# Optimization experiments

Hardware: AMD Instinct MI355X
Metric: run time of the kernel (lower is better)

The kernel has to match this reference:

```python
import jax, jax.numpy as jnp
import numpy as np

ALPHA = 20.0 / 100.0  # dt / tau
ONE_MINUS_ALPHA = 1.0 - ALPHA


def setup_inputs() -> dict:
    key = jax.random.key(0)
    k1, k2, k3 = jax.random.split(key, 3)
    T, B, I, H = 512, 128, 256, 512
    x = jax.random.normal(k1, (T, B, I), dtype=jnp.float32)
    hidden = jnp.zeros((B, H), dtype=jnp.float32)
    # torch Linear weights: [out_features, in_features], scaled like kaiming-uniform-ish
    W_in = jax.random.normal(k2, (H, I), dtype=jnp.float32) / np.sqrt(I)
    W_hh = jax.random.normal(k3, (H, H), dtype=jnp.float32) / np.sqrt(H)
    return {"x": x, "hidden": hidden, "W_in": W_in, "W_hh": W_hh}


def reference(x, hidden, W_in, W_hh):
    # Precompute input projection for all timesteps in one big matmul: [T,B,H]
    xin = jnp.einsum("tbi,hi->tbh", x, W_in)

    def step(h, xin_t):
        pre = xin_t + h @ W_hh.T  # [B,H]
        h_new = jax.nn.relu(h * ONE_MINUS_ALPHA + pre * ALPHA)
        return h_new, h_new

    h_final, output = jax.lax.scan(step, hidden, xin)
    return output, h_final
```

## Files before the change

kernel.cpp:

```cpp
#include <hip/hip_runtime.h>

typedef _Float16 half8 __attribute__((ext_vector_type(8)));
typedef float f32x4 __attribute__((ext_vector_type(4)));

#define NT 512
#define NB 128
#define NI 256
#define NH 512
#define NG 8
#define NS 8
#define FLAG_STRIDE 16

__global__ void w_transform(const float* __restrict__ Whh,
                            const float* __restrict__ Win,
                            _Float16* __restrict__ Wf_hh,
                            _Float16* __restrict__ Wf_in,
                            int* __restrict__ flags) {
  int tid = blockIdx.x * blockDim.x + threadIdx.x;
  if (tid < 32768) {
    int l = tid & 63, b = tid >> 6;
    int tk = b & 15, tn = b >> 4;
    int n = tn * 16 + (l & 15);
    int k = tk * 32 + (l >> 4) * 8;
    const float* src = Whh + (size_t)n * NH + k;
    _Float16* dst = Wf_hh + (size_t)tid * 8;
#pragma unroll
    for (int j = 0; j < 8; ++j) dst[j] = (_Float16)src[j];
  } else if (tid < 32768 + 16384) {
    int t2 = tid - 32768;
    int l = t2 & 63, b = t2 >> 6;
    int tk = b & 7, tn = b >> 3;
    int n = tn * 16 + (l & 15);
    int k = tk * 32 + (l >> 4) * 8;
    const float* src = Win + (size_t)n * NI + k;
    _Float16* dst = Wf_in + (size_t)t2 * 8;
#pragma unroll
    for (int j = 0; j < 8; ++j) dst[j] = (_Float16)src[j];
  } else if (tid < 32768 + 16384 + NG * NS * FLAG_STRIDE) {
    flags[tid - 32768 - 16384] = 0;
  }
}

__global__ __launch_bounds__(256)
void input_proj(const float* __restrict__ x,
                const _Float16* __restrict__ Wf_in,
                float* __restrict__ xin) {
  int lane = threadIdx.x & 63;
  int wv = threadIdx.x >> 6;
  int m0 = blockIdx.x * 16;
  int c = lane & 15, q = lane >> 4;
  int row = m0 + c;

  f32x4 acc[8];
#pragma unroll
  for (int i = 0; i < 8; ++i) acc[i] = (f32x4){0.f, 0.f, 0.f, 0.f};

#pragma unroll
  for (int kc = 0; kc < 8; ++kc) {
    const float4* ap = (const float4*)(x + (size_t)row * NI + kc * 32 + q * 8);
    float4 a0 = ap[0], a1 = ap[1];
    half8 a;
    a[0] = (_Float16)a0.x; a[1] = (_Float16)a0.y;
    a[2] = (_Float16)a0.z; a[3] = (_Float16)a0.w;
    a[4] = (_Float16)a1.x; a[5] = (_Float16)a1.y;
    a[6] = (_Float16)a1.z; a[7] = (_Float16)a1.w;
#pragma unroll
    for (int nt = 0; nt < 8; ++nt) {
      int tn = wv * 8 + nt;
      const half8* bp =
          (const half8*)(Wf_in + (((size_t)(tn * 8 + kc)) * 64 + lane) * 8);
      acc[nt] = __builtin_amdgcn_mfma_f32_16x16x32_f16(a, *bp, acc[nt], 0, 0, 0);
    }
  }
#pragma unroll
  for (int nt = 0; nt < 8; ++nt) {
    int n = wv * 128 + nt * 16 + c;
#pragma unroll
    for (int r = 0; r < 4; ++r) {
      int m = q * 4 + r;
      xin[(size_t)(m0 + m) * NH + n] = acc[nt][r];
    }
  }
}

__global__ __launch_bounds__(256, 1)
void recurrence(float* __restrict__ dout,
                const float* __restrict__ h0,
                const _Float16* __restrict__ Wf,
                _Float16* __restrict__ hbuf,
                int* __restrict__ flags) {
  __shared__ _Float16 h_sh[16][520];
  __shared__ _Float16 h16s[16][72];

  int g = blockIdx.x >> 3, s = blockIdx.x & 7;
  int tid = threadIdx.x, lane = tid & 63, wv = tid >> 6;
  int c = lane & 15, q = lane >> 4;
  int m0 = g * 16;
  int n0 = s * 64;
  int ncol = wv * 16 + c;

  int nt_global = s * 4 + wv;
  half8 bfrag[16];
#pragma unroll
  for (int kc = 0; kc < 16; ++kc)
    bfrag[kc] =
        *(const half8*)(Wf + (((size_t)(nt_global * 16 + kc)) * 64 + lane) * 8);

  float h32r[4];
#pragma unroll
  for (int r = 0; r < 4; ++r)
    h32r[r] = h0[(size_t)(m0 + q * 4 + r) * NH + n0 + ncol];

  for (int i = tid; i < 16 * 512; i += 256) {
    int m = i >> 9, n = i & 511;
    h_sh[m][n] = (_Float16)h0[(size_t)(m0 + m) * NH + n];
  }
  __syncthreads();

  int* fbase = flags + g * NS * FLAG_STRIDE;
  unsigned long long* hb64 = (unsigned long long*)hbuf;

  int cm = tid >> 4, cc = tid & 15;

#pragma unroll 1
  for (int t = 0; t < NT; ++t) {
    const float* xp = dout + ((size_t)t * NB + m0) * NH + n0;
    float xv[4];
#pragma unroll
    for (int r = 0; r < 4; ++r) xv[r] = xp[(size_t)(q * 4 + r) * NH + ncol];

    f32x4 acc0 = (f32x4){0.f, 0.f, 0.f, 0.f};
    f32x4 acc1 = (f32x4){0.f, 0.f, 0.f, 0.f};
#pragma unroll
    for (int kc = 0; kc < 16; kc += 2) {
      half8 a0 = *(const half8*)&h_sh[c][kc * 32 + q * 8];
      half8 a1 = *(const half8*)&h_sh[c][(kc + 1) * 32 + q * 8];
      acc0 = __builtin_amdgcn_mfma_f32_16x16x32_f16(a0, bfrag[kc], acc0, 0, 0, 0);
      acc1 = __builtin_amdgcn_mfma_f32_16x16x32_f16(a1, bfrag[kc + 1], acc1, 0, 0, 0);
    }

#pragma unroll
    for (int r = 0; r < 4; ++r) {
      int m = q * 4 + r;
      float hn = 0.8f * h32r[r] + 0.2f * (xv[r] + acc0[r] + acc1[r]);
      hn = fmaxf(hn, 0.f);
      h32r[r] = hn;
      dout[((size_t)t * NB + m0 + m) * NH + n0 + ncol] = hn;
      h16s[m][ncol] = (_Float16)hn;
      if (t == NT - 1)
        dout[(size_t)NT * NB * NH + (size_t)(m0 + m) * NH + n0 + ncol] = hn;
    }
    if (t == NT - 1) break;

    __syncthreads();

    {
      unsigned long long v = *(const unsigned long long*)&h16s[cm][cc * 4];
      __hip_atomic_store(
          hb64 + ((((size_t)(t & 1) * NB + m0 + cm) * NH + n0 + cc * 4) >> 2),
          v, __ATOMIC_RELAXED, __HIP_MEMORY_SCOPE_AGENT);
    }
    __syncthreads();

    if (tid == 0)
      __hip_atomic_store(&fbase[s * FLAG_STRIDE], t + 1, __ATOMIC_RELAXED,
                         __HIP_MEMORY_SCOPE_AGENT);
    if (wv == 0 && lane < NS) {
      while (__hip_atomic_load(&fbase[lane * FLAG_STRIDE], __ATOMIC_RELAXED,
                               __HIP_MEMORY_SCOPE_AGENT) < t + 1) {
      }
    }
    __syncthreads();

    {
      const unsigned long long* hb =
          hb64 + ((((size_t)(t & 1) * NB + m0) * NH) >> 2);
      unsigned long long v[8];
#pragma unroll
      for (int j = 0; j < 8; ++j) {
        int k = tid + j * 256;
        v[j] = __hip_atomic_load(hb + k, __ATOMIC_RELAXED,
                                 __HIP_MEMORY_SCOPE_AGENT);
      }
#pragma unroll
      for (int j = 0; j < 8; ++j) {
        int k = tid + j * 256;
        int m = k >> 7, o = k & 127;
        *(unsigned long long*)&h_sh[m][o * 4] = v[j];
      }
    }
    __syncthreads();
  }
}

extern "C" void kernel_launch(void* const* d_in, const int* in_sizes, int n_in,
                              void* d_out, int out_size, void* d_ws,
                              size_t ws_size, hipStream_t stream) {
  const float* x      = (const float*)d_in[0];
  const float* hidden = (const float*)d_in[1];
  const float* W_in   = (const float*)d_in[2];
  const float* W_hh   = (const float*)d_in[3];
  float* out = (float*)d_out;

  _Float16* Wf_hh = (_Float16*)d_ws;
  _Float16* Wf_in = Wf_hh + (size_t)NH * NH;
  _Float16* hbuf  = Wf_in;
  int* flags = (int*)((char*)d_ws + (size_t)NH * NH * 2 + (size_t)NH * NI * 2);

  w_transform<<<196, 256, 0, stream>>>(W_hh, W_in, Wf_hh, Wf_in, flags);
  input_proj<<<(NT * NB) / 16, 256, 0, stream>>>(x, Wf_in, out);

  void* args[] = {(void*)&out, (void*)&hidden, (void*)&Wf_hh, (void*)&hbuf,
                  (void*)&flags};
  hipLaunchCooperativeKernel((void*)recurrence, dim3(NG * NS), dim3(256), args,
                             0, stream);
}
```

Before: 1.353 ms.

## Split recurrence across block pairs and overlap partner exchange with local MFMA half

The recurrence now uses 16 blocks of 512 threads, so each batch group is handled by a pair of blocks that each own half the hidden columns, replacing groups of eight blocks. Each step first runs the MFMAs over the block's own half of h, which is already in shared memory, then waits on the partner's flag and pulls only the partner's half through a column-major exchange buffer. This cuts the number of blocks that must synchronise per step and hides part of the flag wait behind local compute. In exchange, each block holds twice as many weight fragments in registers and does more work per step, with fewer blocks active overall.

```diff
diff --git a/kernel.cpp b/kernel.cpp
--- a/kernel.cpp
+++ b/kernel.cpp
@@ -7,8 +7,6 @@
 #define NB 128
 #define NI 256
 #define NH 512
-#define NG 8
-#define NS 8
 #define FLAG_STRIDE 16
 
 __global__ void w_transform(const float* __restrict__ Whh,
@@ -36,7 +34,7 @@
     _Float16* dst = Wf_in + (size_t)t2 * 8;
 #pragma unroll
     for (int j = 0; j < 8; ++j) dst[j] = (_Float16)src[j];
-  } else if (tid < 32768 + 16384 + NG * NS * FLAG_STRIDE) {
+  } else if (tid < 32768 + 16384 + 256) {
     flags[tid - 32768 - 16384] = 0;
   }
 }
@@ -83,113 +81,139 @@
   }
 }
 
-__global__ __launch_bounds__(256, 1)
+__global__ __launch_bounds__(512, 2)
 void recurrence(float* __restrict__ dout,
                 const float* __restrict__ h0,
                 const _Float16* __restrict__ Wf,
-                _Float16* __restrict__ hbuf,
+                unsigned long long* __restrict__ hbuf64,
                 int* __restrict__ flags) {
   __shared__ _Float16 h_sh[16][520];
-  __shared__ _Float16 h16s[16][72];
-
-  int g = blockIdx.x >> 3, s = blockIdx.x & 7;
+
+  int g = blockIdx.x >> 1, s = blockIdx.x & 1;
   int tid = threadIdx.x, lane = tid & 63, wv = tid >> 6;
   int c = lane & 15, q = lane >> 4;
   int m0 = g * 16;
-  int n0 = s * 64;
-  int ncol = wv * 16 + c;
-
-  int nt_global = s * 4 + wv;
-  half8 bfrag[16];
-#pragma unroll
-  for (int kc = 0; kc < 16; ++kc)
-    bfrag[kc] =
-        *(const half8*)(Wf + (((size_t)(nt_global * 16 + kc)) * 64 + lane) * 8);
-
-  float h32r[4];
-#pragma unroll
-  for (int r = 0; r < 4; ++r)
-    h32r[r] = h0[(size_t)(m0 + q * 4 + r) * NH + n0 + ncol];
-
-  for (int i = tid; i < 16 * 512; i += 256) {
-    int m = i >> 9, n = i & 511;
-    h_sh[m][n] = (_Float16)h0[(size_t)(m0 + m) * NH + n];
-  }
+  int sc = s * 256;
+  int P0 = 256 - sc;
+
+  int ntg = s * 16 + wv * 2;
+  half8 bfrag[2][16];
+#pragma unroll
+  for (int nt = 0; nt < 2; ++nt) {
+#pragma unroll
+    for (int kk = 0; kk < 16; ++kk) {
+      int kcg = (kk < 8) ? (s * 8 + kk) : ((8 - s * 8) + (kk - 8));
+      bfrag[nt][kk] =
+          *(const half8*)(Wf + (((size_t)(ntg + nt) * 16 + kcg) * 64 + lane) * 8);
+    }
+  }
+
+  float h32r[2][4];
+#pragma unroll
+  for (int nt = 0; nt < 2; ++nt)
+#pragma unroll
+    for (int r = 0; r < 4; ++r)
+      h32r[nt][r] =
+          h0[(size_t)(m0 + q * 4 + r) * NH + sc + wv * 32 + nt * 16 + c];
+
+  for (int i = tid; i < 16 * 512; i += 512)
+    h_sh[i >> 9][i & 511] = (_Float16)h0[(size_t)(m0 + (i >> 9)) * NH + (i & 511)];
   __syncthreads();
 
-  int* fbase = flags + g * NS * FLAG_STRIDE;
-  unsigned long long* hb64 = (unsigned long long*)hbuf;
-
-  int cm = tid >> 4, cc = tid & 15;
+  unsigned short* hsb = (unsigned short*)&h_sh[0][0];
+  int* fbase = flags + g * 2 * FLAG_STRIDE;
+  int* myflag = fbase + s * FLAG_STRIDE;
+  int* pflag  = fbase + (1 - s) * FLAG_STRIDE;
 
 #pragma unroll 1
   for (int t = 0; t < NT; ++t) {
-    const float* xp = dout + ((size_t)t * NB + m0) * NH + n0;
-    float xv[4];
-#pragma unroll
-    for (int r = 0; r < 4; ++r) xv[r] = xp[(size_t)(q * 4 + r) * NH + ncol];
-
-    f32x4 acc0 = (f32x4){0.f, 0.f, 0.f, 0.f};
-    f32x4 acc1 = (f32x4){0.f, 0.f, 0.f, 0.f};
-#pragma unroll
-    for (int kc = 0; kc < 16; kc += 2) {
-      half8 a0 = *(const half8*)&h_sh[c][kc * 32 + q * 8];
-      half8 a1 = *(const half8*)&h_sh[c][(kc + 1) * 32 + q * 8];
-      acc0 = __builtin_amdgcn_mfma_f32_16x16x32_f16(a0, bfrag[kc], acc0, 0, 0, 0);
-      acc1 = __builtin_amdgcn_mfma_f32_16x16x32_f16(a1, bfrag[kc + 1], acc1, 0, 0, 0);
-    }
-
-#pragma unroll
-    for (int r = 0; r < 4; ++r) {
-      int m = q * 4 + r;
-      float hn = 0.8f * h32r[r] + 0.2f * (xv[r] + acc0[r] + acc1[r]);
-      hn = fmaxf(hn, 0.f);
-      h32r[r] = hn;
-      dout[((size_t)t * NB + m0 + m) * NH + n0 + ncol] = hn;
-      h16s[m][ncol] = (_Float16)hn;
-      if (t == NT - 1)
-        dout[(size_t)NT * NB * NH + (size_t)(m0 + m) * NH + n0 + ncol] = hn;
-    }
-    if (t == NT - 1) break;
-
+    const float* xp = dout + ((size_t)t * NB + m0) * NH + sc;
+    float xv[2][4];
+#pragma unroll
+    for (int nt = 0; nt < 2; ++nt)
+#pragma unroll
+      for (int r = 0; r < 4; ++r)
+        xv[nt][r] = xp[(size_t)(q * 4 + r) * NH + wv * 32 + nt * 16 + c];
+
+    f32x4 acc[2][2];
+#pragma unroll
+    for (int nt = 0; nt < 2; ++nt) {
+      acc[nt][0] = (f32x4){0.f, 0.f, 0.f, 0.f};
+      acc[nt][1] = (f32x4){0.f, 0.f, 0.f, 0.f};
+    }
+#pragma unroll
+    for (int kk = 0; kk < 8; ++kk) {
+      int kcg = s * 8 + kk;
+      half8 a = *(const half8*)&h_sh[c][kcg * 32 + q * 8];
+#pragma unroll
+      for (int nt = 0; nt < 2; ++nt)
+        acc[nt][kk & 1] = __builtin_amdgcn_mfma_f32_16x16x32_f16(
+            a, bfrag[nt][kk], acc[nt][kk & 1], 0, 0, 0);
+    }
+
+    if (t > 0) {
+      while (__hip_atomic_load(pflag, __ATOMIC_RELAXED,
+                               __HIP_MEMORY_SCOPE_AGENT) < t) {
+      }
+      const unsigned long long* pb =
+          hbuf64 + ((size_t)((t - 1) & 1) * NH + P0) * 32 + (m0 >> 2);
+#pragma unroll
+      for (int j = 0; j < 2; ++j) {
+        int k = tid + j * 512;
+        int col = k >> 2, rq = k & 3;
+        unsigned long long v = __hip_atomic_load(
+            pb + (size_t)col * 32 + rq, __ATOMIC_RELAXED,
+            __HIP_MEMORY_SCOPE_AGENT);
+#pragma unroll
+        for (int i = 0; i < 4; ++i)
+          hsb[(size_t)(rq * 4 + i) * 520 + P0 + col] =
+              (unsigned short)(v >> (16 * i));
+      }
+    }
     __syncthreads();
 
-    {
-      unsigned long long v = *(const unsigned long long*)&h16s[cm][cc * 4];
-      __hip_atomic_store(
-          hb64 + ((((size_t)(t & 1) * NB + m0 + cm) * NH + n0 + cc * 4) >> 2),
-          v, __ATOMIC_RELAXED, __HIP_MEMORY_SCOPE_AGENT);
-    }
+#pragma unroll
+    for (int kk = 8; kk < 16; ++kk) {
+      int kcg = (8 - s * 8) + (kk - 8);
+      half8 a = *(const half8*)&h_sh[c][kcg * 32 + q * 8];
+#pragma unroll
+      for (int nt = 0; nt < 2; ++nt)
+        acc[nt][kk & 1] = __builtin_amdgcn_mfma_f32_16x16x32_f16(
+            a, bfrag[nt][kk], acc[nt][kk & 1], 0, 0, 0);
+    }
+
+    bool last = (t == NT - 1);
+    int slotw = t & 1;
+#pragma unroll
+    for (int nt = 0; nt < 2; ++nt) {
+      int ng = sc + wv * 32 + nt * 16 + c;
+      unsigned long long pk = 0;
+#pragma unroll
+      for (int r = 0; r < 4; ++r) {
+        int m = q * 4 + r;
+        float hn = 0.8f * h32r[nt][r] +
+                   0.2f * (xv[nt][r] + acc[nt][0][r] + acc[nt][1][r]);
+        hn = fmaxf(hn, 0.f);
+        h32r[nt][r] = hn;
+        dout[((size_t)t * NB + m0 + m) * NH + ng] = hn;
+        union { _Float16 h; unsigned short u; } cv;
+        cv.h = (_Float16)hn;
+        pk |= (unsigned long long)cv.u << (16 * r);
+        if (!last) h_sh[m][ng] = cv.h;
+        if (last)
+          dout[(size_t)NT * NB * NH + (size_t)(m0 + m) * NH + ng] = hn;
+      }
+      if (!last)
+        __hip_atomic_store(
+            hbuf64 + ((size_t)slotw * NH + ng) * 32 + (m0 >> 2) + q, pk,
+            __ATOMIC_RELAXED, __HIP_MEMORY_SCOPE_AGENT);
+    }
+    if (last) break;
+
     __syncthreads();
-
     if (tid == 0)
-      __hip_atomic_store(&fbase[s * FLAG_STRIDE], t + 1, __ATOMIC_RELAXED,
+      __hip_atomic_store(myflag, t + 1, __ATOMIC_RELAXED,
                          __HIP_MEMORY_SCOPE_AGENT);
-    if (wv == 0 && lane < NS) {
-      while (__hip_atomic_load(&fbase[lane * FLAG_STRIDE], __ATOMIC_RELAXED,
-                               __HIP_MEMORY_SCOPE_AGENT) < t + 1) {
-      }
-    }
-    __syncthreads();
-
-    {
-      const unsigned long long* hb =
-          hb64 + ((((size_t)(t & 1) * NB + m0) * NH) >> 2);
-      unsigned long long v[8];
-#pragma unroll
-      for (int j = 0; j < 8; ++j) {
-        int k = tid + j * 256;
-        v[j] = __hip_atomic_load(hb + k, __ATOMIC_RELAXED,
-                                 __HIP_MEMORY_SCOPE_AGENT);
-      }
-#pragma unroll
-      for (int j = 0; j < 8; ++j) {
-        int k = tid + j * 256;
-        int m = k >> 7, o = k & 127;
-        *(unsigned long long*)&h_sh[m][o * 4] = v[j];
-      }
-    }
-    __syncthreads();
   }
 }
 
@@ -204,7 +228,7 @@
 
   _Float16* Wf_hh = (_Float16*)d_ws;
   _Float16* Wf_in = Wf_hh + (size_t)NH * NH;
-  _Float16* hbuf  = Wf_in;
+  unsigned long long* hbuf = (unsigned long long*)Wf_in;
   int* flags = (int*)((char*)d_ws + (size_t)NH * NH * 2 + (size_t)NH * NI * 2);
 
   w_transform<<<196, 256, 0, stream>>>(W_hh, W_in, Wf_hh, Wf_in, flags);
@@ -212,6 +236,6 @@
 
   void* args[] = {(void*)&out, (void*)&hidden, (void*)&Wf_hh, (void*)&hbuf,
                   (void*)&flags};
-  hipLaunchCooperativeKernel((void*)recurrence, dim3(NG * NS), dim3(256), args,
-                             0, stream);
-}
+  hipLaunchCooperativeKernel((void*)recurrence, dim3(16), dim3(512), args, 0,
+                             stream);
+}
```

Measured after the change: 1.616 ms. +19.4%, slower.

## Drop LDS staging in recurrence; load h fragments directly from global after flag spin

Applied to the files above, without the earlier changes.

Removes the shared-memory staging of the hidden state. Each lane now writes its fp16 outputs straight to the global exchange buffer and reads its MFMA A-fragments directly from global after all threads spin on the group's eight flags. This cuts several __syncthreads and LDS round trips per timestep, and moves the dout stores after the flag publish so they stay off the critical path. The cost is scattered 2-byte atomic stores, all 256 threads polling flags, and redundant global loads of the full h row by each block.

```diff
diff --git a/kernel.cpp b/kernel.cpp
--- a/kernel.cpp
+++ b/kernel.cpp
@@ -7,8 +7,6 @@
 #define NB 128
 #define NI 256
 #define NH 512
-#define NG 8
-#define NS 8
 #define FLAG_STRIDE 16
 
 __global__ void w_transform(const float* __restrict__ Whh,
@@ -36,7 +34,7 @@
     _Float16* dst = Wf_in + (size_t)t2 * 8;
 #pragma unroll
     for (int j = 0; j < 8; ++j) dst[j] = (_Float16)src[j];
-  } else if (tid < 32768 + 16384 + NG * NS * FLAG_STRIDE) {
+  } else {
     flags[tid - 32768 - 16384] = 0;
   }
 }
@@ -87,17 +85,13 @@
 void recurrence(float* __restrict__ dout,
                 const float* __restrict__ h0,
                 const _Float16* __restrict__ Wf,
-                _Float16* __restrict__ hbuf,
+                unsigned long long* __restrict__ hbuf64,
                 int* __restrict__ flags) {
-  __shared__ _Float16 h_sh[16][520];
-  __shared__ _Float16 h16s[16][72];
-
   int g = blockIdx.x >> 3, s = blockIdx.x & 7;
   int tid = threadIdx.x, lane = tid & 63, wv = tid >> 6;
   int c = lane & 15, q = lane >> 4;
   int m0 = g * 16;
-  int n0 = s * 64;
-  int ncol = wv * 16 + c;
+  int ncol = s * 64 + wv * 16 + c;
 
   int nt_global = s * 4 + wv;
   half8 bfrag[16];
@@ -109,87 +103,95 @@
   float h32r[4];
 #pragma unroll
   for (int r = 0; r < 4; ++r)
-    h32r[r] = h0[(size_t)(m0 + q * 4 + r) * NH + n0 + ncol];
-
-  for (int i = tid; i < 16 * 512; i += 256) {
-    int m = i >> 9, n = i & 511;
-    h_sh[m][n] = (_Float16)h0[(size_t)(m0 + m) * NH + n];
-  }
-  __syncthreads();
-
-  int* fbase = flags + g * NS * FLAG_STRIDE;
-  unsigned long long* hb64 = (unsigned long long*)hbuf;
-
-  int cm = tid >> 4, cc = tid & 15;
+    h32r[r] = h0[(size_t)(m0 + q * 4 + r) * NH + ncol];
+
+  unsigned short* hb16 = (unsigned short*)hbuf64;
+  int* fbase = flags + g * 8 * FLAG_STRIDE;
+  int* myflag = fbase + s * FLAG_STRIDE;
 
 #pragma unroll 1
   for (int t = 0; t < NT; ++t) {
-    const float* xp = dout + ((size_t)t * NB + m0) * NH + n0;
+    const float* xp = dout + ((size_t)t * NB + m0) * NH;
     float xv[4];
 #pragma unroll
     for (int r = 0; r < 4; ++r) xv[r] = xp[(size_t)(q * 4 + r) * NH + ncol];
+
+    half8 afrag[16];
+    if (t == 0) {
+      const float* hp = h0 + (size_t)(m0 + c) * NH + q * 8;
+#pragma unroll
+      for (int kc = 0; kc < 16; ++kc) {
+        float4 a0 = ((const float4*)(hp + kc * 32))[0];
+        float4 a1 = ((const float4*)(hp + kc * 32))[1];
+        half8 a;
+        a[0] = (_Float16)a0.x; a[1] = (_Float16)a0.y;
+        a[2] = (_Float16)a0.z; a[3] = (_Float16)a0.w;
+        a[4] = (_Float16)a1.x; a[5] = (_Float16)a1.y;
+        a[6] = (_Float16)a1.z; a[7] = (_Float16)a1.w;
+        afrag[kc] = a;
+      }
+    } else {
+      for (;;) {
+        int mn = 0x7fffffff;
+#pragma unroll
+        for (int j = 0; j < 8; ++j) {
+          int f = __hip_atomic_load(fbase + j * FLAG_STRIDE, __ATOMIC_RELAXED,
+                                    __HIP_MEMORY_SCOPE_AGENT);
+          mn = min(mn, f);
+        }
+        if (mn >= t) break;
+      }
+      const unsigned long long* src =
+          hbuf64 + ((size_t)((t - 1) & 1) * NB + m0 + c) * (NH / 4) + q * 2;
+#pragma unroll
+      for (int kc = 0; kc < 16; ++kc) {
+        union { unsigned long long u[2]; half8 h; } cv;
+        cv.u[0] = __hip_atomic_load(src + kc * 8, __ATOMIC_RELAXED,
+                                    __HIP_MEMORY_SCOPE_AGENT);
+        cv.u[1] = __hip_atomic_load(src + kc * 8 + 1, __ATOMIC_RELAXED,
+                                    __HIP_MEMORY_SCOPE_AGENT);
+        afrag[kc] = cv.h;
+      }
+    }
 
     f32x4 acc0 = (f32x4){0.f, 0.f, 0.f, 0.f};
     f32x4 acc1 = (f32x4){0.f, 0.f, 0.f, 0.f};
 #pragma unroll
     for (int kc = 0; kc < 16; kc += 2) {
-      half8 a0 = *(const half8*)&h_sh[c][kc * 32 + q * 8];
-      half8 a1 = *(const half8*)&h_sh[c][(kc + 1) * 32 + q * 8];
-      acc0 = __builtin_amdgcn_mfma_f32_16x16x32_f16(a0, bfrag[kc], acc0, 0, 0, 0);
-      acc1 = __builtin_amdgcn_mfma_f32_16x16x32_f16(a1, bfrag[kc + 1], acc1, 0, 0, 0);
-    }
-
+      acc0 = __builtin_amdgcn_mfma_f32_16x16x32_f16(afrag[kc], bfrag[kc], acc0, 0, 0, 0);
+      acc1 = __builtin_amdgcn_mfma_f32_16x16x32_f16(afrag[kc + 1], bfrag[kc + 1], acc1, 0, 0, 0);
+    }
+
+    bool last = (t == NT - 1);
+    int slotw = t & 1;
 #pragma unroll
     for (int r = 0; r < 4; ++r) {
-      int m = q * 4 + r;
       float hn = 0.8f * h32r[r] + 0.2f * (xv[r] + acc0[r] + acc1[r]);
       hn = fmaxf(hn, 0.f);
       h32r[r] = hn;
-      dout[((size_t)t * NB + m0 + m) * NH + n0 + ncol] = hn;
-      h16s[m][ncol] = (_Float16)hn;
-      if (t == NT - 1)
-        dout[(size_t)NT * NB * NH + (size_t)(m0 + m) * NH + n0 + ncol] = hn;
-    }
-    if (t == NT - 1) break;
-
-    __syncthreads();
-
-    {
-      unsigned long long v = *(const unsigned long long*)&h16s[cm][cc * 4];
-      __hip_atomic_store(
-          hb64 + ((((size_t)(t & 1) * NB + m0 + cm) * NH + n0 + cc * 4) >> 2),
-          v, __ATOMIC_RELAXED, __HIP_MEMORY_SCOPE_AGENT);
-    }
-    __syncthreads();
-
-    if (tid == 0)
-      __hip_atomic_store(&fbase[s * FLAG_STRIDE], t + 1, __ATOMIC_RELAXED,
-                         __HIP_MEMORY_SCOPE_AGENT);
-    if (wv == 0 && lane < NS) {
-      while (__hip_atomic_load(&fbase[lane * FLAG_STRIDE], __ATOMIC_RELAXED,
-                               __HIP_MEMORY_SCOPE_AGENT) < t + 1) {
-      }
-    }
-    __syncthreads();
-
-    {
-      const unsigned long long* hb =
-          hb64 + ((((size_t)(t & 1) * NB + m0) * NH) >> 2);
-      unsigned long long v[8];
-#pragma unroll
-      for (int j = 0; j < 8; ++j) {
-        int k = tid + j * 256;
-        v[j] = __hip_atomic_load(hb + k, __ATOMIC_RELAXED,
-                                 __HIP_MEMORY_SCOPE_AGENT);
-      }
-#pragma unroll
-      for (int j = 0; j < 8; ++j) {
-        int k = tid + j * 256;
-        int m = k >> 7, o = k & 127;
-        *(unsigned long long*)&h_sh[m][o * 4] = v[j];
-      }
-    }
-    __syncthreads();
+      if (!last) {
+        union { _Float16 h; unsigned short u; } cv;
+        cv.h = (_Float16)hn;
+        __hip_atomic_store(
+            hb16 + ((size_t)slotw * NB + m0 + q * 4 + r) * NH + ncol, cv.u,
+            __ATOMIC_RELAXED, __HIP_MEMORY_SCOPE_AGENT);
+      }
+    }
+
+    if (!last) {
+      __syncthreads();
+      if (tid == 0)
+        __hip_atomic_store(myflag, t + 1, __ATOMIC_RELAXED,
+                           __HIP_MEMORY_SCOPE_AGENT);
+    }
+
+#pragma unroll
+    for (int r = 0; r < 4; ++r) {
+      int m = q * 4 + r;
+      dout[((size_t)t * NB + m0 + m) * NH + ncol] = h32r[r];
+      if (last)
+        dout[(size_t)NT * NB * NH + (size_t)(m0 + m) * NH + ncol] = h32r[r];
+    }
   }
 }
 
@@ -204,7 +206,7 @@
 
   _Float16* Wf_hh = (_Float16*)d_ws;
   _Float16* Wf_in = Wf_hh + (size_t)NH * NH;
-  _Float16* hbuf  = Wf_in;
+  unsigned long long* hbuf = (unsigned long long*)Wf_in;
   int* flags = (int*)((char*)d_ws + (size_t)NH * NH * 2 + (size_t)NH * NI * 2);
 
   w_transform<<<196, 256, 0, stream>>>(W_hh, W_in, Wf_hh, Wf_in, flags);
@@ -212,6 +214,6 @@
 
   void* args[] = {(void*)&out, (void*)&hidden, (void*)&Wf_hh, (void*)&hbuf,
                   (void*)&flags};
-  hipLaunchCooperativeKernel((void*)recurrence, dim3(NG * NS), dim3(256), args,
-                             0, stream);
-}
+  hipLaunchCooperativeKernel((void*)recurrence, dim3(64), dim3(256), args, 0,
+                             stream);
+}
```

Result: slower. 2.656 ms (+96.3%).

## Use per-wave completion flags and drop block barriers in recurrence handoff

Applied to the files above, without the earlier changes.

Each wave now publishes its own flag after draining its hidden-state stores with an explicit vmcnt wait, instead of one flag per block set after two block-wide barriers. Every wave polls all 32 flags of its group with s_sleep backoff, so two __syncthreads per timestep go away. The per-step output store is moved after the flag publish so it overlaps the wait. In exchange, 32 lanes per wave now poll flags packed into one cache line, and correctness depends on the manual waitcnt ordering under relaxed atomics.

```diff
diff --git a/kernel.cpp b/kernel.cpp
--- a/kernel.cpp
+++ b/kernel.cpp
@@ -7,9 +7,6 @@
 #define NB 128
 #define NI 256
 #define NH 512
-#define NG 8
-#define NS 8
-#define FLAG_STRIDE 16
 
 __global__ void w_transform(const float* __restrict__ Whh,
                             const float* __restrict__ Win,
@@ -36,7 +33,7 @@
     _Float16* dst = Wf_in + (size_t)t2 * 8;
 #pragma unroll
     for (int j = 0; j < 8; ++j) dst[j] = (_Float16)src[j];
-  } else if (tid < 32768 + 16384 + NG * NS * FLAG_STRIDE) {
+  } else if (tid < 32768 + 16384 + 256) {
     flags[tid - 32768 - 16384] = 0;
   }
 }
@@ -87,7 +84,7 @@
 void recurrence(float* __restrict__ dout,
                 const float* __restrict__ h0,
                 const _Float16* __restrict__ Wf,
-                _Float16* __restrict__ hbuf,
+                unsigned long long* __restrict__ hbuf64,
                 int* __restrict__ flags) {
   __shared__ _Float16 h_sh[16][520];
   __shared__ _Float16 h16s[16][72];
@@ -117,8 +114,9 @@
   }
   __syncthreads();
 
-  int* fbase = flags + g * NS * FLAG_STRIDE;
-  unsigned long long* hb64 = (unsigned long long*)hbuf;
+  int* fbase = flags + g * 32;
+  int* myflag = fbase + s * 4 + wv;
+  unsigned long long* hb64 = (unsigned long long*)hbuf64;
 
   int cm = tid >> 4, cc = tid & 15;
 
@@ -139,38 +137,48 @@
       acc1 = __builtin_amdgcn_mfma_f32_16x16x32_f16(a1, bfrag[kc + 1], acc1, 0, 0, 0);
     }
 
+    bool last = (t == NT - 1);
 #pragma unroll
     for (int r = 0; r < 4; ++r) {
       int m = q * 4 + r;
       float hn = 0.8f * h32r[r] + 0.2f * (xv[r] + acc0[r] + acc1[r]);
       hn = fmaxf(hn, 0.f);
       h32r[r] = hn;
-      dout[((size_t)t * NB + m0 + m) * NH + n0 + ncol] = hn;
       h16s[m][ncol] = (_Float16)hn;
-      if (t == NT - 1)
-        dout[(size_t)NT * NB * NH + (size_t)(m0 + m) * NH + n0 + ncol] = hn;
-    }
-    if (t == NT - 1) break;
+    }
+
+    if (last) {
+#pragma unroll
+      for (int r = 0; r < 4; ++r) {
+        int m = q * 4 + r;
+        dout[((size_t)t * NB + m0 + m) * NH + n0 + ncol] = h32r[r];
+        dout[(size_t)NT * NB * NH + (size_t)(m0 + m) * NH + n0 + ncol] = h32r[r];
+      }
+      break;
+    }
 
     __syncthreads();
 
-    {
-      unsigned long long v = *(const unsigned long long*)&h16s[cm][cc * 4];
-      __hip_atomic_store(
-          hb64 + ((((size_t)(t & 1) * NB + m0 + cm) * NH + n0 + cc * 4) >> 2),
-          v, __ATOMIC_RELAXED, __HIP_MEMORY_SCOPE_AGENT);
-    }
-    __syncthreads();
-
-    if (tid == 0)
-      __hip_atomic_store(&fbase[s * FLAG_STRIDE], t + 1, __ATOMIC_RELAXED,
+    __hip_atomic_store(
+        hb64 + ((((size_t)(t & 1) * NB + m0 + cm) * NH + n0 + cc * 4) >> 2),
+        *(const unsigned long long*)&h16s[cm][cc * 4],
+        __ATOMIC_RELAXED, __HIP_MEMORY_SCOPE_AGENT);
+
+    asm volatile("s_waitcnt vmcnt(0)" ::: "memory");
+    if (lane == 0)
+      __hip_atomic_store(myflag, t + 1, __ATOMIC_RELAXED,
                          __HIP_MEMORY_SCOPE_AGENT);
-    if (wv == 0 && lane < NS) {
-      while (__hip_atomic_load(&fbase[lane * FLAG_STRIDE], __ATOMIC_RELAXED,
+
+#pragma unroll
+    for (int r = 0; r < 4; ++r)
+      dout[((size_t)t * NB + m0 + q * 4 + r) * NH + n0 + ncol] = h32r[r];
+
+    if (lane < 32) {
+      while (__hip_atomic_load(fbase + lane, __ATOMIC_RELAXED,
                                __HIP_MEMORY_SCOPE_AGENT) < t + 1) {
-      }
-    }
-    __syncthreads();
+        __builtin_amdgcn_s_sleep(1);
+      }
+    }
 
     {
       const unsigned long long* hb =
@@ -204,7 +212,7 @@
 
   _Float16* Wf_hh = (_Float16*)d_ws;
   _Float16* Wf_in = Wf_hh + (size_t)NH * NH;
-  _Float16* hbuf  = Wf_in;
+  unsigned long long* hbuf = (unsigned long long*)Wf_in;
   int* flags = (int*)((char*)d_ws + (size_t)NH * NH * 2 + (size_t)NH * NI * 2);
 
   w_transform<<<196, 256, 0, stream>>>(W_hh, W_in, Wf_hh, Wf_in, flags);
@@ -212,6 +220,6 @@
 
   void* args[] = {(void*)&out, (void*)&hidden, (void*)&Wf_hh, (void*)&hbuf,
                   (void*)&flags};
-  hipLaunchCooperativeKernel((void*)recurrence, dim3(NG * NS), dim3(256), args,
-                             0, stream);
-}
+  hipLaunchCooperativeKernel((void*)recurrence, dim3(64), dim3(256), args, 0,
+                             stream);
+}
```

Result: slower. 1.808 ms (+33.6%).
